# Optimization experiments

Measured on AMD Instinct MI355X. Metric: run time of the kernel, lower is better.

The kernel has to match this reference:

```python
import jax, jax.numpy as jnp
import numpy as np

N_INSTANCES = 32  # instance ids 1..32 assumed present (id 0 = background)


def setup_inputs() -> dict:
    key = jax.random.key(0)
    ks = jax.random.split(key, 6)
    B, F, H, W = 8, 64, 512, 512
    encoded = jax.random.normal(ks[0], (B, F, H, W), dtype=jnp.float32)
    masks = jax.random.randint(ks[1], (B, 1, H, W), 0, N_INSTANCES + 1, dtype=jnp.int32)
    w1 = jax.random.normal(ks[2], (2 * F, F // 2), dtype=jnp.float32) * (1.0 / np.sqrt(2 * F))
    b1 = jax.random.normal(ks[3], (F // 2,), dtype=jnp.float32) * 0.01
    w2 = jax.random.normal(ks[4], (F // 2, 4), dtype=jnp.float32) * (1.0 / np.sqrt(F // 2))
    b2 = jax.random.normal(ks[5], (4,), dtype=jnp.float32) * 0.01
    return {"encoded": encoded, "masks": masks, "w1": w1, "b1": b1, "w2": w2, "b2": b2}


def reference(encoded, masks, w1, b1, w2, b2):
    B, F, H, W = encoded.shape
    N = N_INSTANCES
    ids = masks[:, 0].reshape(B, H * W)                    # [B, HW] int ids 0..N
    feats = jnp.transpose(encoded, (0, 2, 3, 1)).reshape(B, H * W, F)  # [B, HW, F]
    # Original: cur_mask * encoded then max over H,W. Outside-mask pixels contribute 0,
    # so the result equals max(0, segment_max of features over the instance's pixels).
    seg = jax.vmap(lambda f, i: jax.ops.segment_max(f, i, num_segments=N + 1))(feats, ids)
    vectors = jnp.maximum(seg[:, 1:, :], 0.0)              # [B, N, F] (drop background id 0)
    # Pairwise relation MLP: pair(i, j) = concat(v_i, v_j)
    vi = jnp.broadcast_to(vectors[:, :, None, :], (B, N, N, F))
    vj = jnp.broadcast_to(vectors[:, None, :, :], (B, N, N, F))
    pair = jnp.concatenate([vi, vj], axis=-1)              # [B, N(i), N(j), 2F]
    h = jnp.einsum('bijk,kh->bijh', pair, w1) + b1         # [B, N, N, F//2]
    out = jax.nn.sigmoid(jnp.einsum('bijh,hc->bijc', h, w2) + b2)  # [B, N(i), N(j), C]
    # torch layout: connections[b, c, j, i]
    connections = jnp.transpose(out, (0, 3, 2, 1))         # [B, C, N, N]
    return vectors, connections
```

## Files before the change

### kernel.cpp

```cpp
#include <hip/hip_runtime.h>
#include <math.h>

#define HW    (512 * 512)
#define FCH   64
#define NB    8
#define NID   32
#define CHUNK 2048
#define PRIV  (33 * 8)

__global__ __launch_bounds__(512) void segmax_kernel(
    const float* __restrict__ encoded,
    const int*   __restrict__ masks,
    float*       __restrict__ vectors)
{
    const int b      = blockIdx.y;
    const int chunk0 = blockIdx.x * CHUNK;
    const int tid    = threadIdx.x;
    const int wave   = tid >> 6;
    const int lane   = tid & 63;
    const int g      = lane & 7;

    __shared__ int   ids[CHUNK];
    __shared__ float priv[8 * PRIV];

    ((int4*)ids)[tid] = ((const int4*)(masks + (size_t)b * HW + chunk0))[tid];
    __syncthreads();

    float* pw = priv + wave * PRIV;
    const float* ebase = encoded + (size_t)b * FCH * HW + chunk0;
    const float4 z4 = make_float4(0.0f, 0.0f, 0.0f, 0.0f);

    for (int k = 0; k < 8; ++k) {
        const int f = wave * 8 + k;
        const float4* src = (const float4*)(ebase + (size_t)f * HW);

        ((float4*)pw)[lane] = z4;
        if (lane < 2) ((float4*)pw)[64 + lane] = z4;
        asm volatile("s_waitcnt lgkmcnt(0)" ::: "memory");

#pragma unroll
        for (int it = 0; it < CHUNK / 256; ++it) {
            const int idx = it * 64 + lane;
            const float4 v  = src[idx];
            const int4   id = ((const int4*)ids)[idx];
            atomicMax((unsigned*)&pw[(id.x << 3) + g], __float_as_uint(fmaxf(v.x, 0.0f)));
            atomicMax((unsigned*)&pw[(id.y << 3) + g], __float_as_uint(fmaxf(v.y, 0.0f)));
            atomicMax((unsigned*)&pw[(id.z << 3) + g], __float_as_uint(fmaxf(v.z, 0.0f)));
            atomicMax((unsigned*)&pw[(id.w << 3) + g], __float_as_uint(fmaxf(v.w, 0.0f)));
        }
        asm volatile("s_waitcnt lgkmcnt(0)" ::: "memory");

        const float4 m4 = ((const float4*)(pw + 8))[lane];
        float m = fmaxf(fmaxf(m4.x, m4.y), fmaxf(m4.z, m4.w));
        m = fmaxf(m, __shfl_xor(m, 1));
        if ((lane & 1) == 0 && m > 0.0f) {
            atomicMax((unsigned*)&vectors[((size_t)b * NID + (lane >> 1)) * FCH + f],
                      __float_as_uint(m));
        }
        asm volatile("s_waitcnt lgkmcnt(0)" ::: "memory");
    }
}

__global__ __launch_bounds__(256) void conn_kernel(
    const float* __restrict__ vectors,
    const float* __restrict__ w1,
    const float* __restrict__ b1,
    const float* __restrict__ w2,
    const float* __restrict__ b2,
    float*       __restrict__ out)
{
    const int b   = blockIdx.x;
    const int tid = threadIdx.x;

    __shared__ float v[NID][FCH];
    __shared__ float A[FCH][4], Bm[FCH][4];
    __shared__ float s[NID][4], t[NID][4];
    __shared__ float cc[4];

    for (int i = tid; i < NID * FCH; i += 256)
        ((float*)v)[i] = vectors[(size_t)b * NID * FCH + i];

    {
        const int k = tid >> 2, c = tid & 3;
        float a = 0.0f, bb = 0.0f;
#pragma unroll
        for (int h = 0; h < 32; ++h) {
            const float w2v = w2[h * 4 + c];
            a  += w1[k * 32 + h]        * w2v;
            bb += w1[(k + 64) * 32 + h] * w2v;
        }
        A[k][c]  = a;
        Bm[k][c] = bb;
        if (tid < 4) {
            float x = b2[tid];
#pragma unroll
            for (int h = 0; h < 32; ++h) x += b1[h] * w2[h * 4 + tid];
            cc[tid] = x;
        }
    }
    __syncthreads();

    if (tid < 128) {
        const int i = tid >> 2, c = tid & 3;
        float a = 0.0f;
#pragma unroll
        for (int f = 0; f < FCH; ++f) a += v[i][f] * A[f][c];
        s[i][c] = a;
    } else {
        const int j = (tid - 128) >> 2, c = tid & 3;
        float a = 0.0f;
#pragma unroll
        for (int f = 0; f < FCH; ++f) a += v[j][f] * Bm[f][c];
        t[j][c] = a;
    }
    __syncthreads();

    for (int o = tid; o < 4 * NID * NID; o += 256) {
        const int i = o & 31;
        const int j = (o >> 5) & 31;
        const int c = o >> 10;
        const float x = s[i][c] + t[j][c] + cc[c];
        out[(((size_t)b * 4 + c) * NID + j) * NID + i] = 1.0f / (1.0f + expf(-x));
    }
}

extern "C" void kernel_launch(void* const* d_in, const int* in_sizes, int n_in,
                              void* d_out, int out_size, void* d_ws, size_t ws_size,
                              hipStream_t stream) {
    const float* encoded = (const float*)d_in[0];
    const int*   masks   = (const int*)d_in[1];
    const float* w1      = (const float*)d_in[2];
    const float* b1      = (const float*)d_in[3];
    const float* w2      = (const float*)d_in[4];
    const float* b2      = (const float*)d_in[5];
    float* out = (float*)d_out;

    float* vectors     = out;
    float* connections = out + NB * NID * FCH;

    hipMemsetAsync(vectors, 0, (size_t)NB * NID * FCH * sizeof(float), stream);

    segmax_kernel<<<dim3(HW / CHUNK, NB), 512, 0, stream>>>(encoded, masks, vectors);
    conn_kernel<<<NB, 256, 0, stream>>>(vectors, w1, b1, w2, b2, connections);
}
```

Before: 725.0 us.

## Double-buffer encoded loads into LDS via global_load_lds and batch global atomics

The segmax kernel now streams each wave's feature rows into a per-wave double buffer in LDS with async global_load_lds, overlapping the next sub-chunk's fetch with the atomicMax work on the current one. Mask ids are held in registers instead of shared memory, and the private histogram shrinks from 8 to 4 replicas per id to save LDS and zeroing. Per-channel results are collected in LDS and flushed with one batch of global atomics at the end, which removes the per-channel global atomic phase. Occupancy is hinted at 4 blocks per CU. The cost is fewer replicas, so more same-address LDS atomic conflicts, plus heavier register and LDS use and fragile manual waitcnt ordering.

New measurement: 770.4 us. 6.3% more time.

```diff
diff --git a/kernel.cpp b/kernel.cpp
--- a/kernel.cpp
+++ b/kernel.cpp
@@ -6,58 +6,108 @@
 #define NB    8
 #define NID   32
 #define CHUNK 2048
-#define PRIV  (33 * 8)
+#define SUB   1024
+#define NW    8
 
-__global__ __launch_bounds__(512) void segmax_kernel(
+__device__ __forceinline__ void glds16(const float* src, float* dst) {
+    typedef __attribute__((address_space(1))) const void gvoid_t;
+    typedef __attribute__((address_space(3))) void       lvoid_t;
+    __builtin_amdgcn_global_load_lds((gvoid_t*)src, (lvoid_t*)dst, 16, 0, 0);
+}
+
+__device__ __forceinline__ void stage4(const float* gsrc, float* ldst, int lane) {
+#pragma unroll
+    for (int i = 0; i < 4; ++i)
+        glds16(gsrc + i * 256 + lane * 4, ldst + i * 256);
+}
+
+__global__ __launch_bounds__(512, 4) void segmax_kernel(
     const float* __restrict__ encoded,
     const int*   __restrict__ masks,
     float*       __restrict__ vectors)
 {
-    const int b      = blockIdx.y;
-    const int chunk0 = blockIdx.x * CHUNK;
-    const int tid    = threadIdx.x;
-    const int wave   = tid >> 6;
-    const int lane   = tid & 63;
-    const int g      = lane & 7;
+    const int b    = blockIdx.y;
+    const int c0   = blockIdx.x * CHUNK;
+    const int tid  = threadIdx.x;
+    const int w    = tid >> 6;
+    const int lane = tid & 63;
+    const int g4   = lane & 3;
 
-    __shared__ int   ids[CHUNK];
-    __shared__ float priv[8 * PRIV];
+    __shared__ float buf[NW][2][SUB];
+    __shared__ float priv[NW][33 * 4];
+    __shared__ float res[NW][NID][8];
 
-    ((int4*)ids)[tid] = ((const int4*)(masks + (size_t)b * HW + chunk0))[tid];
-    __syncthreads();
+    float*  pw  = priv[w];
+    float4* pw4 = (float4*)pw;
+    const float4 z4 = make_float4(0.f, 0.f, 0.f, 0.f);
 
-    float* pw = priv + wave * PRIV;
-    const float* ebase = encoded + (size_t)b * FCH * HW + chunk0;
-    const float4 z4 = make_float4(0.0f, 0.0f, 0.0f, 0.0f);
+    int4 id4[8];
+    {
+        const int4* msrc = (const int4*)(masks + (size_t)b * HW + c0);
+#pragma unroll
+        for (int it = 0; it < 8; ++it)
+            id4[it] = msrc[it * 64 + lane];
+    }
 
-    for (int k = 0; k < 8; ++k) {
-        const int f = wave * 8 + k;
-        const float4* src = (const float4*)(ebase + (size_t)f * HW);
+    if (lane < 33) pw4[lane] = z4;
+    asm volatile("s_waitcnt lgkmcnt(0)" ::: "memory");
 
-        ((float4*)pw)[lane] = z4;
-        if (lane < 2) ((float4*)pw)[64 + lane] = z4;
-        asm volatile("s_waitcnt lgkmcnt(0)" ::: "memory");
+    const float* ebase = encoded + ((size_t)b * FCH + w * 8) * HW + c0;
+
+    stage4(ebase, buf[w][0], lane);
 
 #pragma unroll
-        for (int it = 0; it < CHUNK / 256; ++it) {
-            const int idx = it * 64 + lane;
-            const float4 v  = src[idx];
-            const int4   id = ((const int4*)ids)[idx];
-            atomicMax((unsigned*)&pw[(id.x << 3) + g], __float_as_uint(fmaxf(v.x, 0.0f)));
-            atomicMax((unsigned*)&pw[(id.y << 3) + g], __float_as_uint(fmaxf(v.y, 0.0f)));
-            atomicMax((unsigned*)&pw[(id.z << 3) + g], __float_as_uint(fmaxf(v.z, 0.0f)));
-            atomicMax((unsigned*)&pw[(id.w << 3) + g], __float_as_uint(fmaxf(v.w, 0.0f)));
+    for (int c = 0; c < 8; ++c) {
+        const float* esrc = ebase + (size_t)c * HW;
+
+        asm volatile("s_waitcnt vmcnt(0)" ::: "memory");
+#pragma unroll
+        for (int i = 0; i < 4; ++i) {
+            const float4 v  = ((const float4*)buf[w][0])[i * 64 + lane];
+            const int4   id = id4[i];
+            atomicMax((unsigned*)&pw[(id.x << 2) + g4], __float_as_uint(fmaxf(v.x, 0.f)));
+            atomicMax((unsigned*)&pw[(id.y << 2) + g4], __float_as_uint(fmaxf(v.y, 0.f)));
+            atomicMax((unsigned*)&pw[(id.z << 2) + g4], __float_as_uint(fmaxf(v.z, 0.f)));
+            atomicMax((unsigned*)&pw[(id.w << 2) + g4], __float_as_uint(fmaxf(v.w, 0.f)));
         }
+        asm volatile("s_waitcnt lgkmcnt(15)" ::: "memory");
+        stage4(esrc + SUB, buf[w][1], lane);
+
+        asm volatile("s_waitcnt vmcnt(0)" ::: "memory");
+#pragma unroll
+        for (int i = 0; i < 4; ++i) {
+            const float4 v  = ((const float4*)buf[w][1])[i * 64 + lane];
+            const int4   id = id4[4 + i];
+            atomicMax((unsigned*)&pw[(id.x << 2) + g4], __float_as_uint(fmaxf(v.x, 0.f)));
+            atomicMax((unsigned*)&pw[(id.y << 2) + g4], __float_as_uint(fmaxf(v.y, 0.f)));
+            atomicMax((unsigned*)&pw[(id.z << 2) + g4], __float_as_uint(fmaxf(v.z, 0.f)));
+            atomicMax((unsigned*)&pw[(id.w << 2) + g4], __float_as_uint(fmaxf(v.w, 0.f)));
+        }
+        asm volatile("s_waitcnt lgkmcnt(15)" ::: "memory");
+        if (c < 7)
+            stage4(esrc + HW, buf[w][0], lane);
+
         asm volatile("s_waitcnt lgkmcnt(0)" ::: "memory");
+        if (lane < NID) {
+            const float4 m4 = pw4[lane + 1];
+            res[w][lane][c] = fmaxf(fmaxf(m4.x, m4.y), fmaxf(m4.z, m4.w));
+        }
+        if (lane < 33) pw4[lane] = z4;
+        asm volatile("s_waitcnt lgkmcnt(0)" ::: "memory");
+    }
 
-        const float4 m4 = ((const float4*)(pw + 8))[lane];
-        float m = fmaxf(fmaxf(m4.x, m4.y), fmaxf(m4.z, m4.w));
-        m = fmaxf(m, __shfl_xor(m, 1));
-        if ((lane & 1) == 0 && m > 0.0f) {
-            atomicMax((unsigned*)&vectors[((size_t)b * NID + (lane >> 1)) * FCH + f],
-                      __float_as_uint(m));
-        }
-        asm volatile("s_waitcnt lgkmcnt(0)" ::: "memory");
+    if (lane < NID) {
+        const float4 r0 = *(const float4*)&res[w][lane][0];
+        const float4 r1 = *(const float4*)&res[w][lane][4];
+        float* vd = vectors + ((size_t)b * NID + lane) * FCH + w * 8;
+        if (r0.x > 0.f) atomicMax((unsigned*)&vd[0], __float_as_uint(r0.x));
+        if (r0.y > 0.f) atomicMax((unsigned*)&vd[1], __float_as_uint(r0.y));
+        if (r0.z > 0.f) atomicMax((unsigned*)&vd[2], __float_as_uint(r0.z));
+        if (r0.w > 0.f) atomicMax((unsigned*)&vd[3], __float_as_uint(r0.w));
+        if (r1.x > 0.f) atomicMax((unsigned*)&vd[4], __float_as_uint(r1.x));
+        if (r1.y > 0.f) atomicMax((unsigned*)&vd[5], __float_as_uint(r1.y));
+        if (r1.z > 0.f) atomicMax((unsigned*)&vd[6], __float_as_uint(r1.z));
+        if (r1.w > 0.f) atomicMax((unsigned*)&vd[7], __float_as_uint(r1.w));
     }
 }
 
```
